# Kernel optimization log

Hardware: AMD Instinct MI355X
Metric: run time of the kernel (lower is better)

Reference implementation:

```python
import jax, jax.numpy as jnp
import numpy as np

D_MODEL = 1024
H = 16
D_K = D_MODEL // H
NEG = -10000.0


def setup_inputs() -> dict:
    key = jax.random.key(0)
    ks = jax.random.split(key, 8)
    B, L = 2, 2048
    q = jax.random.normal(ks[0], (B, L, D_MODEL), dtype=jnp.float32)
    k = jax.random.normal(ks[1], (B, L, D_MODEL), dtype=jnp.float32)
    v = jax.random.normal(ks[2], (B, L, D_MODEL), dtype=jnp.float32)
    mask = jax.random.randint(ks[3], (B, 1, 1, L), 0, 2, dtype=jnp.int32)
    s = 1.0 / np.sqrt(D_MODEL)
    w_q = jax.random.normal(ks[4], (D_MODEL, D_MODEL), dtype=jnp.float32) * s
    w_k = jax.random.normal(ks[5], (D_MODEL, D_MODEL), dtype=jnp.float32) * s
    w_v = jax.random.normal(ks[6], (D_MODEL, D_MODEL), dtype=jnp.float32) * s
    w_o = jax.random.normal(ks[7], (D_MODEL, D_MODEL), dtype=jnp.float32) * s
    return {"q": q, "k": k, "v": v, "mask": mask,
            "w_q": w_q, "w_k": w_k, "w_v": w_v, "w_o": w_o}


def reference(q, k, v, mask, w_q, w_k, w_v, w_o):
    B, Lq, _ = q.shape
    Lk = k.shape[1]
    # projections; nn.Linear applies x @ W.T
    qh = (q @ w_q.T).reshape(B, Lq, H, D_K).transpose(0, 2, 1, 3)  # [B,H,Lq,Dk]
    kh = (k @ w_k.T).reshape(B, Lk, H, D_K).transpose(0, 2, 1, 3)
    vh = (v @ w_v.T).reshape(B, Lk, H, D_K).transpose(0, 2, 1, 3)
    scale = 1.0 / jnp.sqrt(jnp.asarray(D_K, dtype=qh.dtype))
    scores = jnp.einsum("bhqd,bhkd->bhqk", qh, kh) * scale  # [B,H,Lq,Lk]
    scores = jnp.where(mask == 0, jnp.asarray(NEG, scores.dtype), scores)
    attn = jax.nn.softmax(scores, axis=-1)
    out = jnp.einsum("bhqk,bhkd->bhqd", attn, vh)  # [B,H,Lq,Dk]
    out = out.transpose(0, 2, 1, 3).reshape(B, Lq, D_MODEL)
    return out @ w_o.T
```

## Files before the change

### kernel.cpp

```cpp
#include <hip/hip_runtime.h>
#include <hip/hip_bf16.h>


using bf8   = __attribute__((ext_vector_type(8))) short;
using f4    = __attribute__((ext_vector_type(4))) float;
using f16v  = __attribute__((ext_vector_type(16))) float;
using u32x4 = __attribute__((ext_vector_type(4))) unsigned int;

__device__ __forceinline__ short f2bf(float f) {
  unsigned u = __float_as_uint(f);
  u = (u + 0x7FFFu + ((u >> 16) & 1u)) >> 16;
  return (short)(unsigned short)u;
}

__device__ __forceinline__ unsigned cvt_pk_bf16(float lo, float hi) {
  unsigned r;
  asm("v_cvt_pk_bf16_f32 %0, %1, %2" : "=v"(r) : "v"(lo), "v"(hi));
  return r;
}

__device__ __forceinline__ void permswap(unsigned &a, unsigned &b) {
  asm volatile("v_permlane32_swap_b32 %0, %1" : "+v"(a), "+v"(b));
}

template<bool FP32IN, bool HEADOUT>
__device__ __forceinline__ void gemm_body(const void* __restrict__ Ain,
                                          const float* __restrict__ W,
                                          void* __restrict__ Out,
                                          int bm, int bn, float scale)
{
  constexpr int LDT = 40;
  __shared__ short As[2][128 * LDT];
  __shared__ short Ws[2][128 * LDT];

  const int tid  = threadIdx.x;
  const int lane = tid & 63;
  const int wv   = tid >> 6;
  const int wm = wv >> 1, wn = wv & 1;
  const int l15 = lane & 15;
  const int lk8 = (lane >> 4) * 8;

  const f4 fz = {0.f, 0.f, 0.f, 0.f};
  f4 acc[4][4];
  #pragma unroll
  for (int mi = 0; mi < 4; ++mi)
    #pragma unroll
    for (int ni = 0; ni < 4; ++ni) acc[mi][ni] = fz;

  const int arow = tid >> 1;
  const int acol = (tid & 1) * 16;

  float4 ra[4]; float4 rw[4]; bf8 ar[2];

  auto loadA = [&](int kt) {
    if constexpr (FP32IN) {
      const float4* src = (const float4*)((const float*)Ain + (long)(bm + arow) * 1024 + kt + acol);
      #pragma unroll
      for (int j = 0; j < 4; ++j) ra[j] = src[j];
    } else {
      const short* src = (const short*)Ain + (long)(bm + arow) * 1024 + kt + acol;
      ar[0] = *(const bf8*)src;
      ar[1] = *(const bf8*)(src + 8);
    }
  };
  auto loadW = [&](int kt) {
    const float4* src = (const float4*)(W + (long)(bn + arow) * 1024 + kt + acol);
    #pragma unroll
    for (int j = 0; j < 4; ++j) rw[j] = src[j];
  };
  auto writeTile = [&](int buf) {
    short* ap = &As[buf][arow * LDT + acol];
    if constexpr (FP32IN) {
      #pragma unroll
      for (int half = 0; half < 2; ++half) {
        u32x4 pk;
        pk[0] = cvt_pk_bf16(ra[2*half].x,   ra[2*half].y);
        pk[1] = cvt_pk_bf16(ra[2*half].z,   ra[2*half].w);
        pk[2] = cvt_pk_bf16(ra[2*half+1].x, ra[2*half+1].y);
        pk[3] = cvt_pk_bf16(ra[2*half+1].z, ra[2*half+1].w);
        *(bf8*)(ap + 8*half) = __builtin_bit_cast(bf8, pk);
      }
    } else {
      *(bf8*)ap     = ar[0];
      *(bf8*)(ap+8) = ar[1];
    }
    short* wp = &Ws[buf][arow * LDT + acol];
    #pragma unroll
    for (int half = 0; half < 2; ++half) {
      u32x4 pk;
      pk[0] = cvt_pk_bf16(rw[2*half].x,   rw[2*half].y);
      pk[1] = cvt_pk_bf16(rw[2*half].z,   rw[2*half].w);
      pk[2] = cvt_pk_bf16(rw[2*half+1].x, rw[2*half+1].y);
      pk[3] = cvt_pk_bf16(rw[2*half+1].z, rw[2*half+1].w);
      *(bf8*)(wp + 8*half) = __builtin_bit_cast(bf8, pk);
    }
  };

  loadA(0); loadW(0); writeTile(0);
  __syncthreads();

  for (int ktI = 0; ktI < 32; ++ktI) {
    const int cur = ktI & 1;
    if (ktI < 31) { loadA((ktI + 1) * 32); loadW((ktI + 1) * 32); }

    bf8 af[4], bfr[4];
    #pragma unroll
    for (int mi = 0; mi < 4; ++mi)
      af[mi] = *(const bf8*)&As[cur][(wm*64 + mi*16 + l15) * LDT + lk8];
    #pragma unroll
    for (int ni = 0; ni < 4; ++ni)
      bfr[ni] = *(const bf8*)&Ws[cur][(wn*64 + ni*16 + l15) * LDT + lk8];
    #pragma unroll
    for (int mi = 0; mi < 4; ++mi)
      #pragma unroll
      for (int ni = 0; ni < 4; ++ni)
        acc[mi][ni] = __builtin_amdgcn_mfma_f32_16x16x32_bf16(af[mi], bfr[ni], acc[mi][ni], 0, 0, 0);

    if (ktI < 31) writeTile(cur ^ 1);
    __syncthreads();
  }

  #pragma unroll
  for (int mi = 0; mi < 4; ++mi) {
    #pragma unroll
    for (int ni = 0; ni < 4; ++ni) {
      #pragma unroll
      for (int r = 0; r < 4; ++r) {
        int mg = bm + wm*64 + mi*16 + (lane >> 4)*4 + r;
        int ng = bn + wn*64 + ni*16 + l15;
        float val = acc[mi][ni][r] * scale;
        if constexpr (HEADOUT) {
          int b = mg >> 11, l = mg & 2047;
          int h = ng >> 6,  d = ng & 63;
          ((short*)Out)[(((long)(b*16 + h) * 2048 + l) << 6) + d] = f2bf(val);
        } else {
          ((float*)Out)[(long)mg * 1024 + ng] = val;
        }
      }
    }
  }
}

__global__ __launch_bounds__(256)
void qkv_gemm(const float* __restrict__ q, const float* __restrict__ k,
              const float* __restrict__ v, const float* __restrict__ wq,
              const float* __restrict__ wk, const float* __restrict__ wv,
              short* __restrict__ qh, short* __restrict__ kh, short* __restrict__ vh)
{
  const int z = blockIdx.z;
  const float* A = (z == 0) ? q : (z == 1) ? k : v;
  const float* W = (z == 0) ? wq : (z == 1) ? wk : wv;
  short* Out     = (z == 0) ? qh : (z == 1) ? kh : vh;
  const float scale = (z == 0) ? 0.125f : 1.0f;
  gemm_body<true, true>(A, W, Out, blockIdx.x * 128, blockIdx.y * 128, scale);
}

__global__ __launch_bounds__(256)
void out_gemm(const short* __restrict__ att, const float* __restrict__ wo,
              float* __restrict__ out)
{
  gemm_body<false, false>(att, wo, out, blockIdx.x * 128, blockIdx.y * 128, 1.0f);
}

__global__ __launch_bounds__(512, 2)
void attn_fwd(const short* __restrict__ qh, const short* __restrict__ kh,
              const short* __restrict__ vh, const int* __restrict__ mask,
              short* __restrict__ att)
{
  __shared__ short Kb[2][64 * 64];
  __shared__ short Vb[2][64 * 64];
  __shared__ short biasB[2][64];

  const int t = threadIdx.x, lane = t & 63, w = t >> 6;
  const int l31 = lane & 31, hi = lane >> 5;
  const unsigned swz = (unsigned)((l31 & 7) << 4);
  const int bh = blockIdx.y, b = bh >> 4, h = bh & 15;
  const int qrow0 = blockIdx.x * 256 + w * 32;
  const long base = (long)bh * 2048 * 64;

  bf8 qb[4];
  {
    const short* qp = qh + base + (long)(qrow0 + l31) * 64 + hi * 8;
    #pragma unroll
    for (int s = 0; s < 4; ++s) qb[s] = *(const bf8*)(qp + s * 16);
  }
  bf8 qb4;
  #pragma unroll
  for (int i = 0; i < 8; ++i) qb4[i] = 0;
  qb4[0] = hi ? (short)0 : (short)0x3F80;
  bf8 ones;
  #pragma unroll
  for (int i = 0; i < 8; ++i) ones[i] = (l31 == 0) ? (short)0x3F80 : (short)0;

  f16v o0, o1, o2, fz16;
  #pragma unroll
  for (int i = 0; i < 16; ++i) { o0[i] = 0.f; o1[i] = 0.f; o2[i] = 0.f; fz16[i] = 0.f; }

  const int sr = t & 63, c8 = (t >> 6) << 3;
  const short* kgp = kh + base + c8;
  const short* vgp = vh + base + c8;
  const unsigned kwb = (unsigned)(sr * 128 + c8 * 2) ^ ((unsigned)(sr & 7) << 4);

  {
    bf8 kr = *(const bf8*)(kgp + (long)sr * 64);
    bf8 vr = *(const bf8*)(vgp + (long)sr * 64);
    *(bf8*)((char*)Kb[0] + kwb) = kr;
    #pragma unroll
    for (int i = 0; i < 8; ++i) {
      unsigned vb_b = (unsigned)((c8 + i) * 128 + sr * 2) ^ ((unsigned)i << 4);
      *(short*)((char*)Vb[0] + vb_b) = vr[i];
    }
    if (t < 64) biasB[0][t] = mask[b * 2048 + t] ? (short)0 : (short)0xC680;
  }
  __syncthreads();

  for (int it = 0; it < 32; ++it) {
    const int cur = it & 1;
    bf8 kr, vr; int mv = 1;
    if (it < 31) {
      const int kt = (it + 1) * 64;
      kr = *(const bf8*)(kgp + (long)(kt + sr) * 64);
      vr = *(const bf8*)(vgp + (long)(kt + sr) * 64);
      if (t < 64) mv = mask[b * 2048 + kt + t];
    }

    const char* Kc = (const char*)Kb[cur];
    const char* Vc = (const char*)Vb[cur];

    f16v sT[2];
    #pragma unroll
    for (int kb2 = 0; kb2 < 2; ++kb2) {
      bf8 ba;
      #pragma unroll
      for (int i = 0; i < 8; ++i) ba[i] = 0;
      ba[0] = hi ? (short)0 : biasB[cur][kb2 * 32 + l31];
      sT[kb2] = __builtin_amdgcn_mfma_f32_32x32x16_bf16(ba, qb4, fz16, 0, 0, 0);
      #pragma unroll
      for (int s = 0; s < 4; ++s) {
        unsigned ab = (unsigned)((kb2 * 32 + l31) * 128 + s * 32 + hi * 16) ^ swz;
        bf8 ka = *(const bf8*)(Kc + ab);
        sT[kb2] = __builtin_amdgcn_mfma_f32_32x32x16_bf16(ka, qb[s], sT[kb2], 0, 0, 0);
      }
    }

    unsigned Lh[16], Hh[16];
    #pragma unroll
    for (int t2 = 0; t2 < 2; ++t2)
      #pragma unroll
      for (int pi = 0; pi < 8; ++pi) {
        float pe0 = exp2f(sT[t2][2*pi]   * 1.44269504f - 11.5415603f);
        float pe1 = exp2f(sT[t2][2*pi+1] * 1.44269504f - 11.5415603f);
        unsigned pkv = cvt_pk_bf16(pe0, pe1);
        unsigned Lv = pkv, Hv = pkv;
        permswap(Lv, Hv);
        Lh[t2*8 + pi] = Lv; Hh[t2*8 + pi] = Hv;
      }

    #pragma unroll
    for (int t2 = 0; t2 < 2; ++t2)
      #pragma unroll
      for (int sl = 0; sl < 2; ++sl) {
        const int bx = t2*8 + sl*4;
        u32x4 tmp;
        tmp[0] = hi ? Lh[bx+2] : Lh[bx+0];
        tmp[1] = hi ? Lh[bx+3] : Lh[bx+1];
        tmp[2] = hi ? Hh[bx+2] : Hh[bx+0];
        tmp[3] = hi ? Hh[bx+3] : Hh[bx+1];
        bf8 pa = __builtin_bit_cast(bf8, tmp);
        const int sg = t2*2 + sl;
        bf8 v0f = *(const bf8*)(Vc + ((unsigned)((0*32 + l31)*128 + sg*32 + hi*16) ^ swz));
        o0 = __builtin_amdgcn_mfma_f32_32x32x16_bf16(pa, v0f, o0, 0, 0, 0);
        bf8 v1f = *(const bf8*)(Vc + ((unsigned)((1*32 + l31)*128 + sg*32 + hi*16) ^ swz));
        o1 = __builtin_amdgcn_mfma_f32_32x32x16_bf16(pa, v1f, o1, 0, 0, 0);
        o2 = __builtin_amdgcn_mfma_f32_32x32x16_bf16(pa, ones, o2, 0, 0, 0);
      }

    if (it < 31) {
      const int nxt = cur ^ 1;
      *(bf8*)((char*)Kb[nxt] + kwb) = kr;
      #pragma unroll
      for (int i = 0; i < 8; ++i) {
        unsigned vb_b = (unsigned)((c8 + i) * 128 + sr * 2) ^ ((unsigned)i << 4);
        *(short*)((char*)Vb[nxt] + vb_b) = vr[i];
      }
      if (t < 64) biasB[nxt][t] = mv ? (short)0 : (short)0xC680;
    }
    __syncthreads();
  }

  #pragma unroll
  for (int r = 0; r < 16; ++r) {
    int qr = (r & 3) + 8 * (r >> 2) + 4 * hi;
    float ls = __shfl(o2[r], hi << 5);
    float inv = 1.0f / ls;
    long rowb = (long)(b * 2048 + qrow0 + qr) * 1024 + h * 64;
    att[rowb + l31]      = f2bf(o0[r] * inv);
    att[rowb + 32 + l31] = f2bf(o1[r] * inv);
  }
}

extern "C" void kernel_launch(void* const* d_in, const int* in_sizes, int n_in,
                              void* d_out, int out_size, void* d_ws, size_t ws_size,
                              hipStream_t stream) {
  const float* q    = (const float*)d_in[0];
  const float* k    = (const float*)d_in[1];
  const float* v    = (const float*)d_in[2];
  const int*   mask = (const int*)d_in[3];
  const float* w_q  = (const float*)d_in[4];
  const float* w_k  = (const float*)d_in[5];
  const float* w_v  = (const float*)d_in[6];
  const float* w_o  = (const float*)d_in[7];
  float* out = (float*)d_out;

  char* ws = (char*)d_ws;
  const long HSZ = 2L * 16 * 2048 * 64 * sizeof(short);
  short* qh  = (short*)(ws);
  short* kh  = (short*)(ws + HSZ);
  short* vh  = (short*)(ws + 2 * HSZ);
  short* att = (short*)(ws + 3 * HSZ);

  qkv_gemm<<<dim3(32, 8, 3), 256, 0, stream>>>(q, k, v, w_q, w_k, w_v, qh, kh, vh);
  attn_fwd<<<dim3(8, 32), dim3(512), 0, stream>>>(qh, kh, vh, mask, att);
  out_gemm<<<dim3(32, 8), 256, 0, stream>>>(att, w_o, out);
}
```

Before: 156.3 us.

## Double attention KV tile to 128 keys and reorder grid by head

```diff
diff --git a/kernel.cpp b/kernel.cpp
--- a/kernel.cpp
+++ b/kernel.cpp
@@ -167,15 +167,15 @@
               const short* __restrict__ vh, const int* __restrict__ mask,
               short* __restrict__ att)
 {
-  __shared__ short Kb[2][64 * 64];
-  __shared__ short Vb[2][64 * 64];
-  __shared__ short biasB[2][64];
+  __shared__ short Kb[2][128 * 64];
+  __shared__ short Vb[2][64 * 128];
+  __shared__ short biasB[2][128];
 
   const int t = threadIdx.x, lane = t & 63, w = t >> 6;
   const int l31 = lane & 31, hi = lane >> 5;
   const unsigned swz = (unsigned)((l31 & 7) << 4);
-  const int bh = blockIdx.y, b = bh >> 4, h = bh & 15;
-  const int qrow0 = blockIdx.x * 256 + w * 32;
+  const int bh = blockIdx.x, b = bh >> 4, h = bh & 15;
+  const int qrow0 = blockIdx.y * 256 + w * 32;
   const long base = (long)bh * 2048 * 64;
 
   bf8 qb[4];
@@ -202,88 +202,103 @@
   const unsigned kwb = (unsigned)(sr * 128 + c8 * 2) ^ ((unsigned)(sr & 7) << 4);
 
   {
-    bf8 kr = *(const bf8*)(kgp + (long)sr * 64);
-    bf8 vr = *(const bf8*)(vgp + (long)sr * 64);
-    *(bf8*)((char*)Kb[0] + kwb) = kr;
+    bf8 kr  = *(const bf8*)(kgp + (long)sr * 64);
+    bf8 kr2 = *(const bf8*)(kgp + (long)(64 + sr) * 64);
+    bf8 vr  = *(const bf8*)(vgp + (long)sr * 64);
+    bf8 vr2 = *(const bf8*)(vgp + (long)(64 + sr) * 64);
+    *(bf8*)((char*)Kb[0] + kwb)        = kr;
+    *(bf8*)((char*)Kb[0] + kwb + 8192) = kr2;
     #pragma unroll
     for (int i = 0; i < 8; ++i) {
-      unsigned vb_b = (unsigned)((c8 + i) * 128 + sr * 2) ^ ((unsigned)i << 4);
-      *(short*)((char*)Vb[0] + vb_b) = vr[i];
-    }
-    if (t < 64) biasB[0][t] = mask[b * 2048 + t] ? (short)0 : (short)0xC680;
+      unsigned a0 = (unsigned)((c8 + i) * 256 + sr * 2)        ^ ((unsigned)(i & 7) << 4);
+      unsigned a1 = (unsigned)((c8 + i) * 256 + (64 + sr) * 2) ^ ((unsigned)(i & 7) << 4);
+      *(short*)((char*)Vb[0] + a0) = vr[i];
+      *(short*)((char*)Vb[0] + a1) = vr2[i];
+    }
+    if (t < 128) biasB[0][t] = mask[b * 2048 + t] ? (short)0 : (short)0xC680;
   }
   __syncthreads();
 
-  for (int it = 0; it < 32; ++it) {
+  for (int it = 0; it < 16; ++it) {
     const int cur = it & 1;
-    bf8 kr, vr; int mv = 1;
-    if (it < 31) {
-      const int kt = (it + 1) * 64;
-      kr = *(const bf8*)(kgp + (long)(kt + sr) * 64);
-      vr = *(const bf8*)(vgp + (long)(kt + sr) * 64);
-      if (t < 64) mv = mask[b * 2048 + kt + t];
+    bf8 kr, kr2, vr, vr2; int mv = 1;
+    if (it < 15) {
+      const int kt = (it + 1) * 128;
+      kr  = *(const bf8*)(kgp + (long)(kt + sr) * 64);
+      kr2 = *(const bf8*)(kgp + (long)(kt + 64 + sr) * 64);
+      vr  = *(const bf8*)(vgp + (long)(kt + sr) * 64);
+      vr2 = *(const bf8*)(vgp + (long)(kt + 64 + sr) * 64);
+      if (t < 128) mv = mask[b * 2048 + kt + t];
     }
 
     const char* Kc = (const char*)Kb[cur];
     const char* Vc = (const char*)Vb[cur];
 
-    f16v sT[2];
-    #pragma unroll
-    for (int kb2 = 0; kb2 < 2; ++kb2) {
-      bf8 ba;
-      #pragma unroll
-      for (int i = 0; i < 8; ++i) ba[i] = 0;
-      ba[0] = hi ? (short)0 : biasB[cur][kb2 * 32 + l31];
-      sT[kb2] = __builtin_amdgcn_mfma_f32_32x32x16_bf16(ba, qb4, fz16, 0, 0, 0);
-      #pragma unroll
-      for (int s = 0; s < 4; ++s) {
-        unsigned ab = (unsigned)((kb2 * 32 + l31) * 128 + s * 32 + hi * 16) ^ swz;
-        bf8 ka = *(const bf8*)(Kc + ab);
-        sT[kb2] = __builtin_amdgcn_mfma_f32_32x32x16_bf16(ka, qb[s], sT[kb2], 0, 0, 0);
+    #pragma unroll
+    for (int ha = 0; ha < 2; ++ha) {
+      const int ko = ha * 64;
+
+      f16v sT[2];
+      #pragma unroll
+      for (int kb2 = 0; kb2 < 2; ++kb2) {
+        bf8 ba;
+        #pragma unroll
+        for (int i = 0; i < 8; ++i) ba[i] = 0;
+        ba[0] = hi ? (short)0 : biasB[cur][ko + kb2 * 32 + l31];
+        sT[kb2] = __builtin_amdgcn_mfma_f32_32x32x16_bf16(ba, qb4, fz16, 0, 0, 0);
+        #pragma unroll
+        for (int s = 0; s < 4; ++s) {
+          unsigned ab = (unsigned)((ko + kb2 * 32 + l31) * 128 + s * 32 + hi * 16) ^ swz;
+          bf8 ka = *(const bf8*)(Kc + ab);
+          sT[kb2] = __builtin_amdgcn_mfma_f32_32x32x16_bf16(ka, qb[s], sT[kb2], 0, 0, 0);
+        }
       }
-    }
-
-    unsigned Lh[16], Hh[16];
-    #pragma unroll
-    for (int t2 = 0; t2 < 2; ++t2)
-      #pragma unroll
-      for (int pi = 0; pi < 8; ++pi) {
-        float pe0 = exp2f(sT[t2][2*pi]   * 1.44269504f - 11.5415603f);
-        float pe1 = exp2f(sT[t2][2*pi+1] * 1.44269504f - 11.5415603f);
-        unsigned pkv = cvt_pk_bf16(pe0, pe1);
-        unsigned Lv = pkv, Hv = pkv;
-        permswap(Lv, Hv);
-        Lh[t2*8 + pi] = Lv; Hh[t2*8 + pi] = Hv;
+
+      unsigned Lh[16], Hh[16];
+      #pragma unroll
+      for (int t2 = 0; t2 < 2; ++t2)
+        #pragma unroll
+        for (int pi = 0; pi < 8; ++pi) {
+          float pe0 = exp2f(sT[t2][2*pi]   * 1.44269504f - 11.5415603f);
+          float pe1 = exp2f(sT[t2][2*pi+1] * 1.44269504f - 11.5415603f);
+          unsigned pkv = cvt_pk_bf16(pe0, pe1);
+          unsigned Lv = pkv, Hv = pkv;
+          permswap(Lv, Hv);
+          Lh[t2*8 + pi] = Lv; Hh[t2*8 + pi] = Hv;
+        }
+
+      #pragma unroll
+      for (int t2 = 0; t2 < 2; ++t2)
+        #pragma unroll
+        for (int sl = 0; sl < 2; ++sl) {
+          const int bx = t2*8 + sl*4;
+          u32x4 tmp;
+          tmp[0] = hi ? Lh[bx+2] : Lh[bx+0];
+          tmp[1] = hi ? Lh[bx+3] : Lh[bx+1];
+          tmp[2] = hi ? Hh[bx+2] : Hh[bx+0];
+          tmp[3] = hi ? Hh[bx+3] : Hh[bx+1];
+          bf8 pa = __builtin_bit_cast(bf8, tmp);
+          const int sg = t2*2 + sl;
+          bf8 v0f = *(const bf8*)(Vc + ((unsigned)((0*32 + l31)*256 + ko*2 + sg*32 + hi*16) ^ swz));
+          o0 = __builtin_amdgcn_mfma_f32_32x32x16_bf16(pa, v0f, o0, 0, 0, 0);
+          bf8 v1f = *(const bf8*)(Vc + ((unsigned)((1*32 + l31)*256 + ko*2 + sg*32 + hi*16) ^ swz));
+          o1 = __builtin_amdgcn_mfma_f32_32x32x16_bf16(pa, v1f, o1, 0, 0, 0);
+          o2 = __builtin_amdgcn_mfma_f32_32x32x16_bf16(pa, ones, o2, 0, 0, 0);
+        }
+    }
+
+    if (it < 15) {
+      const int nxt = cur ^ 1;
+      *(bf8*)((char*)Kb[nxt] + kwb)        = kr;
+      *(bf8*)((char*)Kb[nxt] + kwb + 8192) = kr2;
+      #pragma unroll
+      for (int i = 0; i < 8; ++i) {
+        unsigned a0 = (unsigned)((c8 + i) * 256 + sr * 2)        ^ ((unsigned)(i & 7) << 4);
+        unsigned a1 = (unsigned)((c8 + i) * 256 + (64 + sr) * 2) ^ ((unsigned)(i & 7) << 4);
+        *(short*)((char*)Vb[nxt] + a0) = vr[i];
+        *(short*)((char*)Vb[nxt] + a1) = vr2[i];
       }
-
-    #pragma unroll
-    for (int t2 = 0; t2 < 2; ++t2)
-      #pragma unroll
-      for (int sl = 0; sl < 2; ++sl) {
-        const int bx = t2*8 + sl*4;
-        u32x4 tmp;
-        tmp[0] = hi ? Lh[bx+2] : Lh[bx+0];
-        tmp[1] = hi ? Lh[bx+3] : Lh[bx+1];
-        tmp[2] = hi ? Hh[bx+2] : Hh[bx+0];
-        tmp[3] = hi ? Hh[bx+3] : Hh[bx+1];
-        bf8 pa = __builtin_bit_cast(bf8, tmp);
-        const int sg = t2*2 + sl;
-        bf8 v0f = *(const bf8*)(Vc + ((unsigned)((0*32 + l31)*128 + sg*32 + hi*16) ^ swz));
-        o0 = __builtin_amdgcn_mfma_f32_32x32x16_bf16(pa, v0f, o0, 0, 0, 0);
-        bf8 v1f = *(const bf8*)(Vc + ((unsigned)((1*32 + l31)*128 + sg*32 + hi*16) ^ swz));
-        o1 = __builtin_amdgcn_mfma_f32_32x32x16_bf16(pa, v1f, o1, 0, 0, 0);
-        o2 = __builtin_amdgcn_mfma_f32_32x32x16_bf16(pa, ones, o2, 0, 0, 0);
-      }
-
-    if (it < 31) {
-      const int nxt = cur ^ 1;
-      *(bf8*)((char*)Kb[nxt] + kwb) = kr;
-      #pragma unroll
-      for (int i = 0; i < 8; ++i) {
-        unsigned vb_b = (unsigned)((c8 + i) * 128 + sr * 2) ^ ((unsigned)i << 4);
-        *(short*)((char*)Vb[nxt] + vb_b) = vr[i];
-      }
-      if (t < 64) biasB[nxt][t] = mv ? (short)0 : (short)0xC680;
+      if (t < 128) biasB[nxt][t] = mv ? (short)0 : (short)0xC680;
     }
     __syncthreads();
   }
@@ -320,6 +335,6 @@
   short* att = (short*)(ws + 3 * HSZ);
 
   qkv_gemm<<<dim3(32, 8, 3), 256, 0, stream>>>(q, k, v, w_q, w_k, w_v, qh, kh, vh);
-  attn_fwd<<<dim3(8, 32), dim3(512), 0, stream>>>(qh, kh, vh, mask, att);
+  attn_fwd<<<dim3(32, 8), dim3(512), 0, stream>>>(qh, kh, vh, mask, att);
   out_gemm<<<dim3(32, 8), 256, 0, stream>>>(att, w_o, out);
 }
```

After: 154.0 us. About the same (-1.5%).

## Split KV sequence across two warp groups in attention and merge partials

Applied to the files above, without the earlier changes.

```diff
diff --git a/kernel.cpp b/kernel.cpp
--- a/kernel.cpp
+++ b/kernel.cpp
@@ -162,20 +162,20 @@
   gemm_body<false, false>(att, wo, out, blockIdx.x * 128, blockIdx.y * 128, 1.0f);
 }
 
-__global__ __launch_bounds__(512, 2)
+__global__ __launch_bounds__(512, 4)
 void attn_fwd(const short* __restrict__ qh, const short* __restrict__ kh,
               const short* __restrict__ vh, const int* __restrict__ mask,
               short* __restrict__ att)
 {
-  __shared__ short Kb[2][64 * 64];
-  __shared__ short Vb[2][64 * 64];
-  __shared__ short biasB[2][64];
+  __shared__ short KVb[8][4096];
+  __shared__ short biasB[2][2][64];
 
   const int t = threadIdx.x, lane = t & 63, w = t >> 6;
   const int l31 = lane & 31, hi = lane >> 5;
   const unsigned swz = (unsigned)((l31 & 7) << 4);
-  const int bh = blockIdx.y, b = bh >> 4, h = bh & 15;
-  const int qrow0 = blockIdx.x * 256 + w * 32;
+  const int grp = w >> 2;
+  const int bh = blockIdx.x, b = bh >> 4, h = bh & 15;
+  const int qrow0 = blockIdx.y * 128 + (w & 3) * 32;
   const long base = (long)bh * 2048 * 64;
 
   bf8 qb[4];
@@ -197,35 +197,49 @@
   for (int i = 0; i < 16; ++i) { o0[i] = 0.f; o1[i] = 0.f; o2[i] = 0.f; fz16[i] = 0.f; }
 
   const int sr = t & 63, c8 = (t >> 6) << 3;
-  const short* kgp = kh + base + c8;
-  const short* vgp = vh + base + c8;
+  const short* kgp0 = kh + base + c8;
+  const short* vgp0 = vh + base + c8;
+  const short* kgp1 = kh + base + (long)1024 * 64 + c8;
+  const short* vgp1 = vh + base + (long)1024 * 64 + c8;
   const unsigned kwb = (unsigned)(sr * 128 + c8 * 2) ^ ((unsigned)(sr & 7) << 4);
 
   {
-    bf8 kr = *(const bf8*)(kgp + (long)sr * 64);
-    bf8 vr = *(const bf8*)(vgp + (long)sr * 64);
-    *(bf8*)((char*)Kb[0] + kwb) = kr;
+    bf8 k0 = *(const bf8*)(kgp0 + (long)sr * 64);
+    bf8 k1 = *(const bf8*)(kgp1 + (long)sr * 64);
+    bf8 v0 = *(const bf8*)(vgp0 + (long)sr * 64);
+    bf8 v1 = *(const bf8*)(vgp1 + (long)sr * 64);
+    *(bf8*)((char*)KVb[0] + kwb) = k0;
+    *(bf8*)((char*)KVb[2] + kwb) = k1;
     #pragma unroll
     for (int i = 0; i < 8; ++i) {
-      unsigned vb_b = (unsigned)((c8 + i) * 128 + sr * 2) ^ ((unsigned)i << 4);
-      *(short*)((char*)Vb[0] + vb_b) = vr[i];
-    }
-    if (t < 64) biasB[0][t] = mask[b * 2048 + t] ? (short)0 : (short)0xC680;
+      unsigned a = (unsigned)((c8 + i) * 128 + sr * 2) ^ ((unsigned)i << 4);
+      *(short*)((char*)KVb[4] + a) = v0[i];
+      *(short*)((char*)KVb[6] + a) = v1[i];
+    }
+    if (t < 64) {
+      biasB[0][0][t] = mask[b * 2048 + t]        ? (short)0 : (short)0xC680;
+      biasB[1][0][t] = mask[b * 2048 + 1024 + t] ? (short)0 : (short)0xC680;
+    }
   }
   __syncthreads();
 
-  for (int it = 0; it < 32; ++it) {
+  for (int it = 0; it < 16; ++it) {
     const int cur = it & 1;
-    bf8 kr, vr; int mv = 1;
-    if (it < 31) {
+    bf8 k0, k1, v0, v1; int mv0 = 1, mv1 = 1;
+    if (it < 15) {
       const int kt = (it + 1) * 64;
-      kr = *(const bf8*)(kgp + (long)(kt + sr) * 64);
-      vr = *(const bf8*)(vgp + (long)(kt + sr) * 64);
-      if (t < 64) mv = mask[b * 2048 + kt + t];
-    }
-
-    const char* Kc = (const char*)Kb[cur];
-    const char* Vc = (const char*)Vb[cur];
+      k0 = *(const bf8*)(kgp0 + (long)(kt + sr) * 64);
+      k1 = *(const bf8*)(kgp1 + (long)(kt + sr) * 64);
+      v0 = *(const bf8*)(vgp0 + (long)(kt + sr) * 64);
+      v1 = *(const bf8*)(vgp1 + (long)(kt + sr) * 64);
+      if (t < 64) {
+        mv0 = mask[b * 2048 + kt + t];
+        mv1 = mask[b * 2048 + 1024 + kt + t];
+      }
+    }
+
+    const char* Kc = (const char*)KVb[grp * 2 + cur];
+    const char* Vc = (const char*)KVb[4 + grp * 2 + cur];
 
     f16v sT[2];
     #pragma unroll
@@ -233,7 +247,7 @@
       bf8 ba;
       #pragma unroll
       for (int i = 0; i < 8; ++i) ba[i] = 0;
-      ba[0] = hi ? (short)0 : biasB[cur][kb2 * 32 + l31];
+      ba[0] = hi ? (short)0 : biasB[grp][cur][kb2 * 32 + l31];
       sT[kb2] = __builtin_amdgcn_mfma_f32_32x32x16_bf16(ba, qb4, fz16, 0, 0, 0);
       #pragma unroll
       for (int s = 0; s < 4; ++s) {
@@ -275,27 +289,52 @@
         o2 = __builtin_amdgcn_mfma_f32_32x32x16_bf16(pa, ones, o2, 0, 0, 0);
       }
 
-    if (it < 31) {
+    if (it < 15) {
       const int nxt = cur ^ 1;
-      *(bf8*)((char*)Kb[nxt] + kwb) = kr;
+      *(bf8*)((char*)KVb[0 + nxt] + kwb) = k0;
+      *(bf8*)((char*)KVb[2 + nxt] + kwb) = k1;
       #pragma unroll
       for (int i = 0; i < 8; ++i) {
-        unsigned vb_b = (unsigned)((c8 + i) * 128 + sr * 2) ^ ((unsigned)i << 4);
-        *(short*)((char*)Vb[nxt] + vb_b) = vr[i];
-      }
-      if (t < 64) biasB[nxt][t] = mv ? (short)0 : (short)0xC680;
+        unsigned a = (unsigned)((c8 + i) * 128 + sr * 2) ^ ((unsigned)i << 4);
+        *(short*)((char*)KVb[4 + nxt] + a) = v0[i];
+        *(short*)((char*)KVb[6 + nxt] + a) = v1[i];
+      }
+      if (t < 64) {
+        biasB[0][nxt][t] = mv0 ? (short)0 : (short)0xC680;
+        biasB[1][nxt][t] = mv1 ? (short)0 : (short)0xC680;
+      }
     }
     __syncthreads();
   }
 
-  #pragma unroll
-  for (int r = 0; r < 16; ++r) {
-    int qr = (r & 3) + 8 * (r >> 2) + 4 * hi;
-    float ls = __shfl(o2[r], hi << 5);
-    float inv = 1.0f / ls;
-    long rowb = (long)(b * 2048 + qrow0 + qr) * 1024 + h * 64;
-    att[rowb + l31]      = f2bf(o0[r] * inv);
-    att[rowb + 32 + l31] = f2bf(o1[r] * inv);
+  float* exch = (float*)&KVb[0][0];
+  if (grp == 1) {
+    float* p = exch + ((w & 3) * 64 + lane) * 48;
+    #pragma unroll
+    for (int j = 0; j < 16; ++j) {
+      p[j]      = o0[j];
+      p[16 + j] = o1[j];
+      p[32 + j] = o2[j];
+    }
+  }
+  __syncthreads();
+  if (grp == 0) {
+    const float* p = exch + ((w & 3) * 64 + lane) * 48;
+    #pragma unroll
+    for (int j = 0; j < 16; ++j) {
+      o0[j] += p[j];
+      o1[j] += p[16 + j];
+      o2[j] += p[32 + j];
+    }
+    #pragma unroll
+    for (int r = 0; r < 16; ++r) {
+      int qr = (r & 3) + 8 * (r >> 2) + 4 * hi;
+      float ls = __shfl(o2[r], hi << 5);
+      float inv = 1.0f / ls;
+      long rowb = (long)(b * 2048 + qrow0 + qr) * 1024 + h * 64;
+      att[rowb + l31]      = f2bf(o0[r] * inv);
+      att[rowb + 32 + l31] = f2bf(o1[r] * inv);
+    }
   }
 }
 
@@ -320,6 +359,6 @@
   short* att = (short*)(ws + 3 * HSZ);
 
   qkv_gemm<<<dim3(32, 8, 3), 256, 0, stream>>>(q, k, v, w_q, w_k, w_v, qh, kh, vh);
-  attn_fwd<<<dim3(8, 32), dim3(512), 0, stream>>>(qh, kh, vh, mask, att);
+  attn_fwd<<<dim3(32, 16), dim3(512), 0, stream>>>(qh, kh, vh, mask, att);
   out_gemm<<<dim3(32, 8), 256, 0, stream>>>(att, w_o, out);
 }
```

After: 271.1 us. 73.5% more time.
